# Kernel tuning notes

Hardware: AMD Instinct MI355X
Metric: run time of the kernel (lower is better)

## Reference

```python
import jax, jax.numpy as jnp
import numpy as np

NUM_ITERATIONS = 3
NUM_ROUTES = 6912  # 32*6*6*6


def _squash(t):
    # t: [..., O]; squash along last dim
    sq = jnp.sum(t * t, axis=-1, keepdims=True)
    return sq * t / ((1.0 + sq) * jnp.sqrt(sq))


def setup_inputs() -> dict:
    key = jax.random.key(0)
    k1, k2 = jax.random.split(key)
    B, R, I, C, O = 64, NUM_ROUTES, 8, 10, 16
    x = jax.random.normal(k1, (B, R, I), dtype=jnp.float32)
    route_weights = jax.random.normal(k2, (C, R, I, O), dtype=jnp.float32)
    return {"x": x, "route_weights": route_weights}


def reference(x, route_weights):
    # x: [B, R, I]; route_weights: [C, R, I, O]
    # priors = x[None,:,:,None,:] @ W[:,None,:,:,:] -> [C, B, R, 1, O]
    priors = jnp.einsum('bri,crio->cbro', x, route_weights)[:, :, :, None, :]
    logits = jnp.zeros_like(priors)  # [C, B, R, 1, O]
    outputs = None
    for i in range(NUM_ITERATIONS):
        # softmax over routes (dim=2), matching custom softmax(input, dim=2)
        probs = jax.nn.softmax(logits, axis=2)
        outputs = _squash(jnp.sum(probs * priors, axis=2, keepdims=True))  # [C,B,1,1,O]
        if i != NUM_ROUTES - 1:  # always true in original (num_routes >> iters)
            delta = jnp.sum(priors * outputs, axis=-1, keepdims=True)  # [C,B,R,1,1]
            logits = logits + delta
    return outputs
```

## Files before the change

kernel.cpp:

```cpp
#include <hip/hip_runtime.h>
#include <math.h>

#define BB 64
#define RR 6912
#define II 8
#define CC 10
#define OO 16
#define RPB 64
#define NCH 108
#define NIT 8
#define LDSF 4608

typedef _Float16 h2 __attribute__((ext_vector_type(2)));
union HV { int4 v; h2 h[4]; };

__global__ __launch_bounds__(256) void transpose_cvt_kernel(
    const float* __restrict__ x, int4* __restrict__ xth4)
{
    __shared__ float4 lds4[64 * 34];
    const int rblk = blockIdx.x >> 2;
    const int bblk = blockIdx.x & 3;
    const int r0 = rblk * 64, b0 = bblk * 16;
    const int t = threadIdx.x;
    {
        const int rl = t & 63;
        const int bl0 = t >> 6;
#pragma unroll
        for (int kb = 0; kb < 4; ++kb) {
            const int bl = kb * 4 + bl0;
            const float4* src = (const float4*)(x + ((size_t)(b0 + bl) * RR + (r0 + rl)) * II);
            lds4[rl * 34 + bl * 2 + 0] = src[0];
            lds4[rl * 34 + bl * 2 + 1] = src[1];
        }
    }
    __syncthreads();
    {
        const int bl = t & 15;
        const int rw0 = t >> 4;
#pragma unroll
        for (int kr = 0; kr < 4; ++kr) {
            const int rw = kr * 16 + rw0;
            float4 a = lds4[rw * 34 + bl * 2 + 0];
            float4 bq = lds4[rw * 34 + bl * 2 + 1];
            HV u;
            u.h[0] = h2{(_Float16)a.x,  (_Float16)a.y};
            u.h[1] = h2{(_Float16)a.z,  (_Float16)a.w};
            u.h[2] = h2{(_Float16)bq.x, (_Float16)bq.y};
            u.h[3] = h2{(_Float16)bq.z, (_Float16)bq.w};
            xth4[(size_t)(r0 + rw) * BB + (b0 + bl)] = u.v;
        }
    }
}

__global__ __launch_bounds__(256) void wcvt_kernel(
    const float4* __restrict__ w4, int4* __restrict__ wh4)
{
    __shared__ __align__(16) _Float16 wl[1024];
    const int blk = blockIdx.x;
    const int t = threadIdx.x;
    const float4 v = w4[(size_t)blk * 256 + t];
    const int rp = t >> 5;
    const int i  = (t >> 2) & 7;
    const int o0 = (t & 3) * 4;
    wl[(rp * 16 + o0 + 0) * 8 + i] = (_Float16)v.x;
    wl[(rp * 16 + o0 + 1) * 8 + i] = (_Float16)v.y;
    wl[(rp * 16 + o0 + 2) * 8 + i] = (_Float16)v.z;
    wl[(rp * 16 + o0 + 3) * 8 + i] = (_Float16)v.w;
    __syncthreads();
    if (t < 128) wh4[(size_t)blk * 128 + t] = ((const int4*)wl)[t];
}

template <int MODE>
__global__ __launch_bounds__(256, 4) void pass_kernel(
    const int4* __restrict__ xth4, const int4* __restrict__ wh4,
    const float* __restrict__ ov_in,
    float* __restrict__ pacc, float* __restrict__ pz)
{
    __shared__ __align__(16) float lds[LDSF];
    int4* wlds = (int4*)lds;

    const int bid = blockIdx.x;
    const int c = bid / NCH;
    const int chunk = bid - c * NCH;
    const int t = threadIdx.x;
    const int wv = t >> 6;
    const int lane = t & 63;
    const int rr = lane >> 5;
    const int bg = lane & 31;

    {
        const int4* src = wh4 + (size_t)(c * (RR / 8) + chunk * 8) * 128;
#pragma unroll
        for (int k = 0; k < 4; ++k) wlds[k * 256 + t] = src[k * 256 + t];
    }

    float acc0[OO], acc1[OO];
#pragma unroll
    for (int o = 0; o < OO; ++o) { acc0[o] = 0.f; acc1[o] = 0.f; }
    float Z0 = 0.f, Z1 = 0.f;

    float ov0[OO], ov1[OO];
    if (MODE != 0) {
        const float4* opa = (const float4*)(ov_in + ((size_t)c * BB + bg) * OO);
        const float4* opb = (const float4*)(ov_in + ((size_t)c * BB + bg + 32) * OO);
#pragma unroll
        for (int q = 0; q < 4; ++q) {
            float4 va = opa[q], vb = opb[q];
            ov0[q*4+0]=va.x; ov0[q*4+1]=va.y; ov0[q*4+2]=va.z; ov0[q*4+3]=va.w;
            ov1[q*4+0]=vb.x; ov1[q*4+1]=vb.y; ov1[q*4+2]=vb.z; ov1[q*4+3]=vb.w;
        }
    }

    __syncthreads();

#pragma unroll 1
    for (int it = 0; it < NIT; ++it) {
        const int rl = it * 8 + wv * 2 + rr;
        const int r  = chunk * RPB + rl;
        HV xa, xb;
        xa.v = xth4[(size_t)r * BB + bg];
        xb.v = xth4[(size_t)r * BB + bg + 32];

        float p0[OO], p1[OO];
#pragma unroll
        for (int o = 0; o < OO; ++o) {
            HV wq; wq.v = wlds[rl * 16 + o];
            float a = __builtin_amdgcn_fdot2(xa.h[0], wq.h[0],
                        (MODE == 0) ? acc0[o] : 0.f, false);
            a = __builtin_amdgcn_fdot2(xa.h[1], wq.h[1], a, false);
            a = __builtin_amdgcn_fdot2(xa.h[2], wq.h[2], a, false);
            a = __builtin_amdgcn_fdot2(xa.h[3], wq.h[3], a, false);
            float bb = __builtin_amdgcn_fdot2(xb.h[0], wq.h[0],
                        (MODE == 0) ? acc1[o] : 0.f, false);
            bb = __builtin_amdgcn_fdot2(xb.h[1], wq.h[1], bb, false);
            bb = __builtin_amdgcn_fdot2(xb.h[2], wq.h[2], bb, false);
            bb = __builtin_amdgcn_fdot2(xb.h[3], wq.h[3], bb, false);
            if (MODE == 0) { acc0[o] = a; acc1[o] = bb; }
            else           { p0[o] = a;   p1[o] = bb; }
        }

        if (MODE != 0) {
            float d0 = 0.f, d1 = 0.f;
#pragma unroll
            for (int o = 0; o < OO; ++o) { d0 = fmaf(p0[o], ov0[o], d0); d1 = fmaf(p1[o], ov1[o], d1); }
            const float e0 = __expf(d0), e1 = __expf(d1);
            Z0 += e0; Z1 += e1;
#pragma unroll
            for (int o = 0; o < OO; ++o) { acc0[o] = fmaf(e0, p0[o], acc0[o]); acc1[o] = fmaf(e1, p1[o], acc1[o]); }
        }
    }

#pragma unroll
    for (int o = 0; o < OO; ++o) {
        acc0[o] += __shfl_xor(acc0[o], 32);
        acc1[o] += __shfl_xor(acc1[o], 32);
    }
    if (MODE != 0) { Z0 += __shfl_xor(Z0, 32); Z1 += __shfl_xor(Z1, 32); }

    __syncthreads();
    if (rr == 0) {
        float* s = lds + (wv * 32 + bg) * 36;
#pragma unroll
        for (int o = 0; o < OO; ++o) { s[o] = acc0[o]; s[16 + o] = acc1[o]; }
        s[32] = Z0; s[33] = Z1;
    }
    __syncthreads();

    {
        const int b = t >> 2, q = t & 3;
        const int k = b >> 5, bgf = b & 31;
        float4 sum = make_float4(0.f, 0.f, 0.f, 0.f);
#pragma unroll
        for (int w2 = 0; w2 < 4; ++w2) {
            const float4 v = *(const float4*)(lds + (w2 * 32 + bgf) * 36 + k * 16 + q * 4);
            sum.x += v.x; sum.y += v.y; sum.z += v.z; sum.w += v.w;
        }
        *(float4*)(pacc + (((size_t)(c * NCH + chunk) * BB + b) * OO) + q * 4) = sum;
        if (MODE != 0 && q == 0) {
            float z = 0.f;
#pragma unroll
            for (int w2 = 0; w2 < 4; ++w2) z += lds[(w2 * 32 + bgf) * 36 + 32 + k];
            pz[(size_t)(c * NCH + chunk) * BB + b] = z;
        }
    }
}

template <int MODE>
__global__ __launch_bounds__(256) void combine_kernel(
    const float* __restrict__ pacc, const float* __restrict__ pz,
    const float* __restrict__ out0, float* __restrict__ outw)
{
    __shared__ float lsum[256];
    __shared__ float lz[16];
    const int cb = blockIdx.x;
    const int c = cb >> 6, b = cb & 63;
    const int t = threadIdx.x;
    const int o = t & 15, g = t >> 4;

    float s = 0.f, zl = 0.f;
    for (int p = g; p < NCH; p += 16) {
        s += pacc[((size_t)(c * NCH + p) * BB + b) * OO + o];
        if (MODE != 0 && o == 0) zl += pz[(size_t)(c * NCH + p) * BB + b];
    }
    lsum[t] = s;
    if (MODE != 0 && o == 0) lz[g] = zl;
    __syncthreads();

    if (g == 0) {
#pragma unroll
        for (int k = 1; k < 16; ++k) s += lsum[k * 16 + o];
        if (MODE != 0) {
            float Zt = 0.f;
#pragma unroll
            for (int k = 0; k < 16; ++k) Zt += lz[k];
            s /= Zt;
        } else {
            s *= (1.0f / RR);
        }
        float sq = s * s;
#pragma unroll
        for (int w = 1; w < 16; w <<= 1) sq += __shfl_xor(sq, w);
        float val = s * sqrtf(sq) / (1.f + sq);
        if (MODE == 1) val += out0[(size_t)cb * OO + o];
        outw[(size_t)cb * OO + o] = val;
    }
}

extern "C" void kernel_launch(void* const* d_in, const int* in_sizes, int n_in,
                              void* d_out, int out_size, void* d_ws, size_t ws_size,
                              hipStream_t stream)
{
    const float* x = (const float*)d_in[0];
    const float* w = (const float*)d_in[1];
    float* out = (float*)d_out;

    float* ws = (float*)d_ws;
    float* xth    = ws;
    float* wh     = xth + (size_t)RR * BB * 4;
    float* pacc   = wh + (size_t)CC * RR * 64;
    float* pz     = pacc + (size_t)CC * NCH * BB * OO;
    float* out0   = pz + (size_t)CC * NCH * BB;
    float* outsum = out0 + CC * BB * OO;

    int4* xth4 = (int4*)xth;
    int4* wh4  = (int4*)wh;
    const float4* w4 = (const float4*)w;

    transpose_cvt_kernel<<<dim3((RR / 64) * 4), dim3(256), 0, stream>>>(x, xth4);
    wcvt_kernel<<<dim3(CC * (RR / 8)), dim3(256), 0, stream>>>(w4, wh4);

    const dim3 gp(CC * NCH), bp(256);
    const dim3 gc(CC * BB), bc(256);

    pass_kernel<0><<<gp, bp, 0, stream>>>(xth4, wh4, nullptr, pacc, pz);
    combine_kernel<0><<<gc, bc, 0, stream>>>(pacc, pz, nullptr, out0);
    pass_kernel<1><<<gp, bp, 0, stream>>>(xth4, wh4, out0, pacc, pz);
    combine_kernel<1><<<gc, bc, 0, stream>>>(pacc, pz, out0, outsum);
    pass_kernel<2><<<gp, bp, 0, stream>>>(xth4, wh4, outsum, pacc, pz);
    combine_kernel<2><<<gc, bc, 0, stream>>>(pacc, pz, nullptr, out);
}
```

Measured before the change: 166.9 us.

## Compute priors with 32x32x16 MFMA instead of fdot2 in pass kernel

Replaces the per-lane fdot2 prior computation with MFMA 32x32x16 f16 instructions. Each instruction handles two routes at once, with half the A operand zeroed to select the route. The kernel also prefetches the next x rows to overlap loads with compute. Blocks are remapped so that the capsule dimension varies fastest across neighbouring block ids. The LDS merge layout is reorganized to match the MFMA output fragment layout, which adds cross-lane shuffles to reduce the softmax logits.

```diff
diff --git a/kernel.cpp b/kernel.cpp
--- a/kernel.cpp
+++ b/kernel.cpp
@@ -8,11 +8,14 @@
 #define OO 16
 #define RPB 64
 #define NCH 108
-#define NIT 8
-#define LDSF 4608
+#define NGRP 8
+#define MRG_PAD 20
+#define LDSF (4*64*MRG_PAD + 4*64)
 
 typedef _Float16 h2 __attribute__((ext_vector_type(2)));
-union HV { int4 v; h2 h[4]; };
+typedef _Float16 half8 __attribute__((ext_vector_type(8)));
+typedef float f32x16 __attribute__((ext_vector_type(16)));
+union HV { int4 v; h2 h[4]; half8 h8; };
 
 __global__ __launch_bounds__(256) void transpose_cvt_kernel(
     const float* __restrict__ x, int4* __restrict__ xth4)
@@ -80,13 +83,17 @@
     int4* wlds = (int4*)lds;
 
     const int bid = blockIdx.x;
-    const int c = bid / NCH;
-    const int chunk = bid - c * NCH;
+    const int w = (bid & 7) * 135 + (bid >> 3);
+    const int chunk = w / 10;
+    const int c = w - chunk * 10;
+
     const int t = threadIdx.x;
     const int wv = t >> 6;
-    const int lane = t & 63;
-    const int rr = lane >> 5;
-    const int bg = lane & 31;
+    const int l = t & 63;
+    const int b = l & 31;
+    const int hi = l >> 5;
+    const int aquad = (l >> 4) & 1;
+    const bool aact = (aquad == hi);
 
     {
         const int4* src = wh4 + (size_t)(c * (RR / 8) + chunk * 8) * 128;
@@ -94,93 +101,124 @@
         for (int k = 0; k < 4; ++k) wlds[k * 256 + t] = src[k * 256 + t];
     }
 
-    float acc0[OO], acc1[OO];
-#pragma unroll
-    for (int o = 0; o < OO; ++o) { acc0[o] = 0.f; acc1[o] = 0.f; }
-    float Z0 = 0.f, Z1 = 0.f;
-
-    float ov0[OO], ov1[OO];
+    float accA[8], accB[8];
+#pragma unroll
+    for (int j = 0; j < 8; ++j) { accA[j] = 0.f; accB[j] = 0.f; }
+    float ZA = 0.f, ZB = 0.f;
+
+    float ovA[8], ovB[8];
     if (MODE != 0) {
-        const float4* opa = (const float4*)(ov_in + ((size_t)c * BB + bg) * OO);
-        const float4* opb = (const float4*)(ov_in + ((size_t)c * BB + bg + 32) * OO);
-#pragma unroll
-        for (int q = 0; q < 4; ++q) {
-            float4 va = opa[q], vb = opb[q];
-            ov0[q*4+0]=va.x; ov0[q*4+1]=va.y; ov0[q*4+2]=va.z; ov0[q*4+3]=va.w;
-            ov1[q*4+0]=vb.x; ov1[q*4+1]=vb.y; ov1[q*4+2]=vb.z; ov1[q*4+3]=vb.w;
-        }
-    }
-
-    __syncthreads();
+        const float* pa = ov_in + ((size_t)c * BB + b) * OO + 4 * hi;
+        const float* pb = ov_in + ((size_t)c * BB + 32 + b) * OO + 4 * hi;
+        float4 a0 = *(const float4*)(pa);
+        float4 a1 = *(const float4*)(pa + 8);
+        float4 b0 = *(const float4*)(pb);
+        float4 b1 = *(const float4*)(pb + 8);
+        ovA[0]=a0.x; ovA[1]=a0.y; ovA[2]=a0.z; ovA[3]=a0.w;
+        ovA[4]=a1.x; ovA[5]=a1.y; ovA[6]=a1.z; ovA[7]=a1.w;
+        ovB[0]=b0.x; ovB[1]=b0.y; ovB[2]=b0.z; ovB[3]=b0.w;
+        ovB[4]=b1.x; ovB[5]=b1.y; ovB[6]=b1.z; ovB[7]=b1.w;
+    }
+
+    __syncthreads();
+
+    const int rbase = chunk * RPB + wv * 16;
+
+    f32x16 cA, cB;
+#pragma unroll
+    for (int q = 0; q < 16; ++q) { cA[q] = 0.f; cB[q] = 0.f; }
+
+    HV xc0, xc1, xn0, xn1;
+    xc0.v = xth4[(size_t)(rbase + hi) * BB + b];
+    xc1.v = xth4[(size_t)(rbase + hi) * BB + 32 + b];
+    xn0 = xc0; xn1 = xc1;
 
 #pragma unroll 1
-    for (int it = 0; it < NIT; ++it) {
-        const int rl = it * 8 + wv * 2 + rr;
-        const int r  = chunk * RPB + rl;
-        HV xa, xb;
-        xa.v = xth4[(size_t)r * BB + bg];
-        xb.v = xth4[(size_t)r * BB + bg + 32];
-
-        float p0[OO], p1[OO];
-#pragma unroll
-        for (int o = 0; o < OO; ++o) {
-            HV wq; wq.v = wlds[rl * 16 + o];
-            float a = __builtin_amdgcn_fdot2(xa.h[0], wq.h[0],
-                        (MODE == 0) ? acc0[o] : 0.f, false);
-            a = __builtin_amdgcn_fdot2(xa.h[1], wq.h[1], a, false);
-            a = __builtin_amdgcn_fdot2(xa.h[2], wq.h[2], a, false);
-            a = __builtin_amdgcn_fdot2(xa.h[3], wq.h[3], a, false);
-            float bb = __builtin_amdgcn_fdot2(xb.h[0], wq.h[0],
-                        (MODE == 0) ? acc1[o] : 0.f, false);
-            bb = __builtin_amdgcn_fdot2(xb.h[1], wq.h[1], bb, false);
-            bb = __builtin_amdgcn_fdot2(xb.h[2], wq.h[2], bb, false);
-            bb = __builtin_amdgcn_fdot2(xb.h[3], wq.h[3], bb, false);
-            if (MODE == 0) { acc0[o] = a; acc1[o] = bb; }
-            else           { p0[o] = a;   p1[o] = bb; }
-        }
-
-        if (MODE != 0) {
-            float d0 = 0.f, d1 = 0.f;
-#pragma unroll
-            for (int o = 0; o < OO; ++o) { d0 = fmaf(p0[o], ov0[o], d0); d1 = fmaf(p1[o], ov1[o], d1); }
-            const float e0 = __expf(d0), e1 = __expf(d1);
-            Z0 += e0; Z1 += e1;
-#pragma unroll
-            for (int o = 0; o < OO; ++o) { acc0[o] = fmaf(e0, p0[o], acc0[o]); acc1[o] = fmaf(e1, p1[o], acc1[o]); }
-        }
-    }
-
-#pragma unroll
-    for (int o = 0; o < OO; ++o) {
-        acc0[o] += __shfl_xor(acc0[o], 32);
-        acc1[o] += __shfl_xor(acc1[o], 32);
-    }
-    if (MODE != 0) { Z0 += __shfl_xor(Z0, 32); Z1 += __shfl_xor(Z1, 32); }
-
-    __syncthreads();
-    if (rr == 0) {
-        float* s = lds + (wv * 32 + bg) * 36;
-#pragma unroll
-        for (int o = 0; o < OO; ++o) { s[o] = acc0[o]; s[16 + o] = acc1[o]; }
-        s[32] = Z0; s[33] = Z1;
-    }
-    __syncthreads();
-
-    {
-        const int b = t >> 2, q = t & 3;
-        const int k = b >> 5, bgf = b & 31;
+    for (int g = 0; g < NGRP; ++g) {
+        if (g + 1 < NGRP) {
+            const int rn = rbase + (g + 1) * 2 + hi;
+            xn0.v = xth4[(size_t)rn * BB + b];
+            xn1.v = xth4[(size_t)rn * BB + 32 + b];
+        }
+        const int rl0 = wv * 16 + g * 2;
+        HV wq;
+        wq.v = wlds[(rl0 + aquad) * 16 + (l & 15)];
+        if (!aact) wq.v = make_int4(0, 0, 0, 0);
+
+        if (MODE == 0) {
+            cA = __builtin_amdgcn_mfma_f32_32x32x16_f16(wq.h8, xc0.h8, cA, 0, 0, 0);
+            cB = __builtin_amdgcn_mfma_f32_32x32x16_f16(wq.h8, xc1.h8, cB, 0, 0, 0);
+        } else {
+            f32x16 p0, p1;
+#pragma unroll
+            for (int q = 0; q < 16; ++q) { p0[q] = 0.f; p1[q] = 0.f; }
+            p0 = __builtin_amdgcn_mfma_f32_32x32x16_f16(wq.h8, xc0.h8, p0, 0, 0, 0);
+            p1 = __builtin_amdgcn_mfma_f32_32x32x16_f16(wq.h8, xc1.h8, p1, 0, 0, 0);
+
+            float dA0 = 0.f, dA1 = 0.f, dB0 = 0.f, dB1 = 0.f;
+#pragma unroll
+            for (int j = 0; j < 8; ++j) {
+                dA0 = fmaf(p0[j],     ovA[j], dA0);
+                dA1 = fmaf(p0[j + 8], ovA[j], dA1);
+                dB0 = fmaf(p1[j],     ovB[j], dB0);
+                dB1 = fmaf(p1[j + 8], ovB[j], dB1);
+            }
+            dA0 += __shfl_xor(dA0, 32);
+            dA1 += __shfl_xor(dA1, 32);
+            dB0 += __shfl_xor(dB0, 32);
+            dB1 += __shfl_xor(dB1, 32);
+            const float eA0 = __expf(dA0), eA1 = __expf(dA1);
+            const float eB0 = __expf(dB0), eB1 = __expf(dB1);
+            ZA += eA0 + eA1; ZB += eB0 + eB1;
+#pragma unroll
+            for (int j = 0; j < 8; ++j) {
+                accA[j] = fmaf(eA0, p0[j], fmaf(eA1, p0[j + 8], accA[j]));
+                accB[j] = fmaf(eB0, p1[j], fmaf(eB1, p1[j + 8], accB[j]));
+            }
+        }
+        xc0 = xn0; xc1 = xn1;
+    }
+
+    if (MODE == 0) {
+#pragma unroll
+        for (int j = 0; j < 8; ++j) {
+            accA[j] = cA[j] + cA[j + 8];
+            accB[j] = cB[j] + cB[j + 8];
+        }
+    }
+
+    __syncthreads();
+
+    {
+        float* m0 = lds + (wv * 64 + b) * MRG_PAD + 4 * hi;
+        *(float4*)(m0)     = make_float4(accA[0], accA[1], accA[2], accA[3]);
+        *(float4*)(m0 + 8) = make_float4(accA[4], accA[5], accA[6], accA[7]);
+        float* m1 = lds + (wv * 64 + 32 + b) * MRG_PAD + 4 * hi;
+        *(float4*)(m1)     = make_float4(accB[0], accB[1], accB[2], accB[3]);
+        *(float4*)(m1 + 8) = make_float4(accB[4], accB[5], accB[6], accB[7]);
+        if (MODE != 0 && hi == 0) {
+            float* zr = lds + 4 * 64 * MRG_PAD;
+            zr[wv * 64 + b] = ZA;
+            zr[wv * 64 + 32 + b] = ZB;
+        }
+    }
+    __syncthreads();
+
+    {
+        const int b2 = t >> 2, q = t & 3;
         float4 sum = make_float4(0.f, 0.f, 0.f, 0.f);
 #pragma unroll
         for (int w2 = 0; w2 < 4; ++w2) {
-            const float4 v = *(const float4*)(lds + (w2 * 32 + bgf) * 36 + k * 16 + q * 4);
+            const float4 v = *(const float4*)(lds + (w2 * 64 + b2) * MRG_PAD + q * 4);
             sum.x += v.x; sum.y += v.y; sum.z += v.z; sum.w += v.w;
         }
-        *(float4*)(pacc + (((size_t)(c * NCH + chunk) * BB + b) * OO) + q * 4) = sum;
+        *(float4*)(pacc + (((size_t)(c * NCH + chunk) * BB + b2) * OO) + q * 4) = sum;
         if (MODE != 0 && q == 0) {
+            const float* zr = lds + 4 * 64 * MRG_PAD;
             float z = 0.f;
 #pragma unroll
-            for (int w2 = 0; w2 < 4; ++w2) z += lds[(w2 * 32 + bgf) * 36 + 32 + k];
-            pz[(size_t)(c * NCH + chunk) * BB + b] = z;
+            for (int w2 = 0; w2 < 4; ++w2) z += zr[w2 * 64 + b2];
+            pz[(size_t)(c * NCH + chunk) * BB + b2] = z;
         }
     }
 }
```

Measured after the change: 136.5 us. -18.2%, faster.
